# Performance work log

Measured on AMD Instinct MI355X. Metric: run time of the kernel, lower is better.

## Reference

```python
import jax, jax.numpy as jnp
import numpy as np

IN_F = 256
OUT_F = 256
ALPHA = 0.2  # leakyrelu negative slope


def setup_inputs() -> dict:
    key = jax.random.key(0)
    k1, k2, k3 = jax.random.split(key, 3)
    B, N = 64, 1024
    x_loc = jax.random.normal(k1, (B, N, IN_F), dtype=jnp.float32)
    # xavier_uniform with gain=1.414
    def xavier(k, shape, gain=1.414):
        fan_in, fan_out = shape[0], shape[1]
        bound = gain * np.sqrt(6.0 / (fan_in + fan_out))
        return jax.random.uniform(k, shape, jnp.float32, -bound, bound)
    W = xavier(k2, (IN_F, OUT_F))
    a = xavier(k3, (2 * OUT_F, 1))
    return {"x_loc": x_loc, "W": W, "a": a, "entity_num": N}


def reference(x_loc, W, a, entity_num):
    # h: [B, N, F]
    h = jnp.matmul(x_loc, W)
    F_out = W.shape[1]
    a1 = a[:F_out, 0]   # [F]
    a2 = a[F_out:, 0]   # [F]
    # score(i, j) = leakyrelu(a1 . h_i + a2 . h_j)  -- decomposition of
    # matmul(cat(h_i, h_j), a); identical math, avoids O(N^2 * 2F) tensor.
    s1 = jnp.einsum('bnf,f->bn', h, a1)  # [B, N]
    s2 = jnp.einsum('bnf,f->bn', h, a2)  # [B, N]
    e = s1[:, :, None] + s2[:, None, :]  # [B, N, N]
    e = jnp.where(e > 0, e, ALPHA * e)   # leakyrelu(alpha=0.2)
    attention = jax.nn.softmax(e, axis=2)
    h_prime = jnp.matmul(attention, h)   # [B, N, F]
    return h_prime  # concat=False -> no elu
```

## Files before the change

kernel.cpp:

```cpp
#include <hip/hip_runtime.h>


typedef unsigned short u16;
typedef unsigned int   u32;
typedef float  f32x4  __attribute__((ext_vector_type(4)));
typedef __bf16 bf16x8 __attribute__((ext_vector_type(8)));
typedef __bf16 bf16x4 __attribute__((ext_vector_type(4)));

#define NB    64
#define NENT  1024
#define FD    256
#define NROWS (NB * NENT)
#define ALPHA 0.2f

typedef __attribute__((address_space(1))) const void* gas_ptr;
typedef __attribute__((address_space(3))) void*       las_ptr;
__device__ __forceinline__ void gload16(const void* g, void* l) {
  __builtin_amdgcn_global_load_lds((gas_ptr)g, (las_ptr)l, 16, 0, 0);
}

__global__ __launch_bounds__(256) void k_wa(const float* __restrict__ W,
                                            const float* __restrict__ a,
                                            float* __restrict__ Wa1,
                                            float* __restrict__ Wa2) {
  const int k = blockIdx.x, f = threadIdx.x;
  const float w = W[(size_t)k * FD + f];
  float p1 = w * a[f];
  float p2 = w * a[FD + f];
#pragma unroll
  for (int off = 1; off < 64; off <<= 1) {
    p1 += __shfl_xor(p1, off, 64);
    p2 += __shfl_xor(p2, off, 64);
  }
  __shared__ float r1[4], r2[4];
  const int wv = f >> 6, lane = f & 63;
  if (lane == 0) { r1[wv] = p1; r2[wv] = p2; }
  __syncthreads();
  if (f == 0) {
    Wa1[k] = r1[0] + r1[1] + r1[2] + r1[3];
    Wa2[k] = r2[0] + r2[1] + r2[2] + r2[3];
  }
}

__global__ __launch_bounds__(256) void k_wt(const float* __restrict__ W,
                                            u16* __restrict__ Wt) {
  __shared__ float tile[64][65];
  const int t = threadIdx.x;
  const int ki = blockIdx.x >> 2, fi = blockIdx.x & 3;
  const int k0 = ki * 64, f0 = fi * 64;
  const int r = t >> 4, c4 = (t & 15) * 4;
#pragma unroll
  for (int it = 0; it < 4; ++it) {
    const int row = r + it * 16;
    float4 v = *(const float4*)&W[(size_t)(k0 + row) * FD + f0 + c4];
    tile[row][c4 + 0] = v.x; tile[row][c4 + 1] = v.y;
    tile[row][c4 + 2] = v.z; tile[row][c4 + 3] = v.w;
  }
  __syncthreads();
#pragma unroll
  for (int it = 0; it < 4; ++it) {
    const int fr = r + it * 16;
    bf16x4 pk;
    pk[0] = (__bf16)tile[c4 + 0][fr]; pk[1] = (__bf16)tile[c4 + 1][fr];
    pk[2] = (__bf16)tile[c4 + 2][fr]; pk[3] = (__bf16)tile[c4 + 3][fr];
    *(bf16x4*)&Wt[(size_t)(f0 + fr) * FD + k0 + c4] = pk;
  }
}

__global__ __launch_bounds__(512, 2) void k_h(
    const float* __restrict__ x, const u16* __restrict__ Wt,
    const float* __restrict__ Wa1g, const float* __restrict__ Wa2g,
    u16* __restrict__ h_oct, float* __restrict__ s1, float* __restrict__ s2) {
  __shared__ __align__(16) u16 A_lds[2][4][128][8];
  __shared__ __align__(16) u16 B_lds[2][4][256][8];
  __shared__ float wa1[FD], wa2[FD];
  const int t = threadIdx.x;
  const int lane = t & 63, wv = t >> 6;
  const int wr = wv >> 2, wc = wv & 3;
  const int g16 = lane >> 4, c15 = lane & 15;
  const int rT = blockIdx.x * 128;
  if (t < FD) { wa1[t] = Wa1g[t]; wa2[t] = Wa2g[t]; }
  const int srow = t >> 2, spart = t & 3;
  const float* xsrc = x + (size_t)(rT + srow) * FD + spart * 8;
  float p1 = 0.f, p2 = 0.f;
  f32x4 acc[4][4];
  const f32x4 vz = {0.f, 0.f, 0.f, 0.f};
#pragma unroll
  for (int i = 0; i < 4; ++i)
#pragma unroll
    for (int j = 0; j < 4; ++j) acc[i][j] = vz;

  auto stage = [&](int nb, int kc, const float4& f0, const float4& f1) {
    const int k0n = kc * 32;
    const int d0 = t;
    gload16(Wt + (size_t)(d0 & 255) * FD + k0n + (d0 >> 8) * 8,
            (char*)(&B_lds[nb][0][0][0]) + d0 * 16);
    const int d1 = t + 512;
    gload16(Wt + (size_t)(d1 & 255) * FD + k0n + (d1 >> 8) * 8,
            (char*)(&B_lds[nb][0][0][0]) + d1 * 16);
    bf16x8 aw;
    aw[0] = (__bf16)f0.x; aw[1] = (__bf16)f0.y;
    aw[2] = (__bf16)f0.z; aw[3] = (__bf16)f0.w;
    aw[4] = (__bf16)f1.x; aw[5] = (__bf16)f1.y;
    aw[6] = (__bf16)f1.z; aw[7] = (__bf16)f1.w;
    *(bf16x8*)&A_lds[nb][spart][srow][0] = aw;
    const int kb = k0n + spart * 8;
    p1 += f0.x*wa1[kb+0] + f0.y*wa1[kb+1] + f0.z*wa1[kb+2] + f0.w*wa1[kb+3]
        + f1.x*wa1[kb+4] + f1.y*wa1[kb+5] + f1.z*wa1[kb+6] + f1.w*wa1[kb+7];
    p2 += f0.x*wa2[kb+0] + f0.y*wa2[kb+1] + f0.z*wa2[kb+2] + f0.w*wa2[kb+3]
        + f1.x*wa2[kb+4] + f1.y*wa2[kb+5] + f1.z*wa2[kb+6] + f1.w*wa2[kb+7];
  };
  auto mfma_step = [&](int cb) {
    bf16x8 af[4], bfv[4];
#pragma unroll
    for (int fi = 0; fi < 4; ++fi)
      af[fi] = *(const bf16x8*)&A_lds[cb][g16][wr * 64 + fi * 16 + c15][0];
#pragma unroll
    for (int fj = 0; fj < 4; ++fj)
      bfv[fj] = *(const bf16x8*)&B_lds[cb][g16][wc * 64 + fj * 16 + c15][0];
#pragma unroll
    for (int fi = 0; fi < 4; ++fi)
#pragma unroll
      for (int fj = 0; fj < 4; ++fj)
        acc[fi][fj] = __builtin_amdgcn_mfma_f32_16x16x32_bf16(
            af[fi], bfv[fj], acc[fi][fj], 0, 0, 0);
  };

  float4 xc0 = *(const float4*)(xsrc + 0);
  float4 xc1 = *(const float4*)(xsrc + 4);
  float4 xb0 = *(const float4*)(xsrc + 32);
  float4 xb1 = *(const float4*)(xsrc + 36);
  float4 xa0 = *(const float4*)(xsrc + 64);
  float4 xa1 = *(const float4*)(xsrc + 68);
  __syncthreads();
  stage(0, 0, xc0, xc1);
  __syncthreads();
#pragma unroll 1
  for (int ks2 = 0; ks2 < 4; ++ks2) {
    stage(1, 2 * ks2 + 1, xb0, xb1);
    if (2 * ks2 + 3 < 8) {
      xb0 = *(const float4*)(xsrc + (2 * ks2 + 3) * 32);
      xb1 = *(const float4*)(xsrc + (2 * ks2 + 3) * 32 + 4);
    }
    mfma_step(0);
    __syncthreads();
    if (2 * ks2 + 2 < 8) {
      stage(0, 2 * ks2 + 2, xa0, xa1);
      if (2 * ks2 + 4 < 8) {
        xa0 = *(const float4*)(xsrc + (2 * ks2 + 4) * 32);
        xa1 = *(const float4*)(xsrc + (2 * ks2 + 4) * 32 + 4);
      }
    }
    mfma_step(1);
    __syncthreads();
  }
  p1 += __shfl_xor(p1, 1, 64); p1 += __shfl_xor(p1, 2, 64);
  p2 += __shfl_xor(p2, 1, 64); p2 += __shfl_xor(p2, 2, 64);
  if (spart == 0) { s1[rT + srow] = p1; s2[rT + srow] = p2; }
#pragma unroll
  for (int fi = 0; fi < 4; ++fi) {
    const int rowb = rT + wr * 64 + fi * 16 + 4 * g16;
    const int oct = rowb >> 3, u = rowb & 7;
#pragma unroll
    for (int fj = 0; fj < 4; ++fj) {
      const int col = wc * 64 + fj * 16 + c15;
      bf16x4 pk;
      pk[0] = (__bf16)acc[fi][fj][0]; pk[1] = (__bf16)acc[fi][fj][1];
      pk[2] = (__bf16)acc[fi][fj][2]; pk[3] = (__bf16)acc[fi][fj][3];
      *(bf16x4*)((u16*)h_oct + ((size_t)oct * FD + col) * 8 + u) = pk;
    }
  }
}

__global__ __launch_bounds__(512, 2) void k_pv(
    const u16* __restrict__ h_oct, const float* __restrict__ s1,
    const float* __restrict__ s2, float* __restrict__ out) {
  __shared__ __align__(16) u16 P_lds[2][4][128][8];
  __shared__ __align__(16) u16 V_lds[2][4][256][8];
  __shared__ float s2l[NENT];
  const int t = threadIdx.x;
  const int lane = t & 63, wv = t >> 6;
  const int wr = wv >> 2, wc = wv & 3;
  const int g16 = lane >> 4, c15 = lane & 15;
  const int p = blockIdx.x;
  const int lb = (p & 7) * 64 + (p >> 3);
  const int b = lb >> 3, itile = lb & 7;
  const int i0 = itile * 128;
  const int irow = t & 127, gsl = t >> 7;
  const int rowg = b * NENT + i0 + irow;
  const float s1v = s1[rowg];
  const size_t obase = (size_t)b * (NENT / 8);
  f32x4 acc[4][4];
  const f32x4 vz = {0.f, 0.f, 0.f, 0.f};
#pragma unroll
  for (int i = 0; i < 4; ++i)
#pragma unroll
    for (int j = 0; j < 4; ++j) acc[i][j] = vz;
  float zsum = 0.f;

  auto vload = [&](int nb, int ksn) {
    const int j0n = ksn * 32;
    const int d0 = t;
    gload16(h_oct + ((obase + (j0n >> 3) + (d0 >> 8)) * FD + (d0 & 255)) * 8,
            (char*)(&V_lds[nb][0][0][0]) + d0 * 16);
    const int d1 = t + 512;
    gload16(h_oct + ((obase + (j0n >> 3) + (d1 >> 8)) * FD + (d1 & 255)) * 8,
            (char*)(&V_lds[nb][0][0][0]) + d1 * 16);
  };

  vload(0, 0);
  *(float2*)&s2l[t * 2] = *(const float2*)&s2[(size_t)b * NENT + t * 2];
  __syncthreads();
  float sm = s2l[lane];
#pragma unroll
  for (int j = 1; j < 16; ++j) sm = fmaxf(sm, s2l[lane + j * 64]);
#pragma unroll
  for (int off = 1; off < 64; off <<= 1) sm = fmaxf(sm, __shfl_xor(sm, off, 64));
  const float q = s1v + sm;
  const float mv = fmaxf(q, ALPHA * q);

  auto genp = [&](int nb, int ksn) {
    const int jb = ksn * 32 + gsl * 8;
    bf16x8 pw;
    float zp = 0.f;
#pragma unroll
    for (int u = 0; u < 8; ++u) {
      float z = s1v + s2l[jb + u];
      float l = fmaxf(z, ALPHA * z);
      float pe = __expf(l - mv);
      zp += pe;
      pw[u] = (__bf16)pe;
    }
    zsum += zp;
    *(bf16x8*)&P_lds[nb][gsl][irow][0] = pw;
  };
  auto mfma_step = [&](int cb) {
    bf16x8 af[4], bfv[4];
#pragma unroll
    for (int fi = 0; fi < 4; ++fi)
      af[fi] = *(const bf16x8*)&P_lds[cb][g16][wr * 64 + fi * 16 + c15][0];
#pragma unroll
    for (int fj = 0; fj < 4; ++fj)
      bfv[fj] = *(const bf16x8*)&V_lds[cb][g16][wc * 64 + fj * 16 + c15][0];
#pragma unroll
    for (int fi = 0; fi < 4; ++fi)
#pragma unroll
      for (int fj = 0; fj < 4; ++fj)
        acc[fi][fj] = __builtin_amdgcn_mfma_f32_16x16x32_bf16(
            af[fi], bfv[fj], acc[fi][fj], 0, 0, 0);
  };

  genp(0, 0);
  __syncthreads();
#pragma unroll 1
  for (int ks2 = 0; ks2 < 16; ++ks2) {
    vload(1, 2 * ks2 + 1);
    genp(1, 2 * ks2 + 1);
    mfma_step(0);
    __syncthreads();
    if (2 * ks2 + 2 < 32) {
      vload(0, 2 * ks2 + 2);
      genp(0, 2 * ks2 + 2);
    }
    mfma_step(1);
    __syncthreads();
  }
  float* zred = (float*)&P_lds[0][0][0][0];
  zred[gsl * 128 + irow] = zsum;
  __syncthreads();
#pragma unroll
  for (int fi = 0; fi < 4; ++fi) {
    const int rowb = wr * 64 + fi * 16 + 4 * g16;
    float rz[4];
#pragma unroll
    for (int r = 0; r < 4; ++r)
      rz[r] = 1.0f / (zred[rowb + r] + zred[128 + rowb + r] +
                      zred[256 + rowb + r] + zred[384 + rowb + r]);
#pragma unroll
    for (int fj = 0; fj < 4; ++fj) {
      const int col = wc * 64 + fj * 16 + c15;
      float* o = out + ((size_t)b * NENT + i0 + rowb) * FD + col;
      o[0 * FD] = acc[fi][fj][0] * rz[0];
      o[1 * FD] = acc[fi][fj][1] * rz[1];
      o[2 * FD] = acc[fi][fj][2] * rz[2];
      o[3 * FD] = acc[fi][fj][3] * rz[3];
    }
  }
}

extern "C" void kernel_launch(void* const* d_in, const int* in_sizes, int n_in,
                              void* d_out, int out_size, void* d_ws, size_t ws_size,
                              hipStream_t stream) {
  const float* x = (const float*)d_in[0];
  const float* W = (const float*)d_in[1];
  const float* a = (const float*)d_in[2];
  float* out = (float*)d_out;

  char* ws = (char*)d_ws;
  u16*   h_oct = (u16*)ws;
  float* s1  = (float*)(ws + (size_t)33554432);
  float* s2  = s1 + NROWS;
  float* Wa1 = s2 + NROWS;
  float* Wa2 = Wa1 + FD;
  u16*   Wt  = (u16*)(Wa2 + FD);

  k_wa<<<dim3(256), dim3(256), 0, stream>>>(W, a, Wa1, Wa2);
  k_wt<<<dim3(16), dim3(256), 0, stream>>>(W, Wt);
  k_h<<<dim3(NROWS / 128), dim3(512), 0, stream>>>(x, Wt, Wa1, Wa2, h_oct, s1, s2);
  k_pv<<<dim3(NB * 8), dim3(512), 0, stream>>>(h_oct, s1, s2, out);
}
```

Baseline: 81.88 us.

## Double row tile to 256 in both GEMM kernels and use exp2-based softmax

Both k_h and k_pv now process 256 rows per block instead of 128, so each wave computes an 8x4 MFMA tile. This halves how often the W and V tiles are reloaded per output row and shrinks the grid to 256 blocks. The softmax generation in k_pv folds leakyrelu into a max of two FMAs followed by a raw v_exp_f32, and reads s2 with vector LDS loads. The larger accumulators raise register pressure, and the 256-block grid may leave compute units underused on a 256-CU device at 2 blocks per CU.

```diff
diff --git a/kernel.cpp b/kernel.cpp
--- a/kernel.cpp
+++ b/kernel.cpp
@@ -12,11 +12,17 @@
 #define FD    256
 #define NROWS (NB * NENT)
 #define ALPHA 0.2f
+#define LOG2E 1.4426950408889634f
 
 typedef __attribute__((address_space(1))) const void* gas_ptr;
 typedef __attribute__((address_space(3))) void*       las_ptr;
 __device__ __forceinline__ void gload16(const void* g, void* l) {
   __builtin_amdgcn_global_load_lds((gas_ptr)g, (las_ptr)l, 16, 0, 0);
+}
+__device__ __forceinline__ float fexp2(float x) {
+  float r;
+  asm("v_exp_f32 %0, %1" : "=v"(r) : "v"(x));
+  return r;
 }
 
 __global__ __launch_bounds__(256) void k_wa(const float* __restrict__ W,
@@ -71,26 +77,29 @@
     const float* __restrict__ x, const u16* __restrict__ Wt,
     const float* __restrict__ Wa1g, const float* __restrict__ Wa2g,
     u16* __restrict__ h_oct, float* __restrict__ s1, float* __restrict__ s2) {
-  __shared__ __align__(16) u16 A_lds[2][4][128][8];
+  __shared__ __align__(16) u16 A_lds[2][4][256][8];
   __shared__ __align__(16) u16 B_lds[2][4][256][8];
   __shared__ float wa1[FD], wa2[FD];
   const int t = threadIdx.x;
   const int lane = t & 63, wv = t >> 6;
   const int wr = wv >> 2, wc = wv & 3;
   const int g16 = lane >> 4, c15 = lane & 15;
-  const int rT = blockIdx.x * 128;
+  const int p = blockIdx.x;
+  const int lb = (p & 7) * 32 + (p >> 3);
+  const int rT = lb * 256;
   if (t < FD) { wa1[t] = Wa1g[t]; wa2[t] = Wa2g[t]; }
-  const int srow = t >> 2, spart = t & 3;
-  const float* xsrc = x + (size_t)(rT + srow) * FD + spart * 8;
+  const int row = t >> 1, half = t & 1;
+  const float* xsrc = x + (size_t)(rT + row) * FD + half * 16;
   float p1 = 0.f, p2 = 0.f;
-  f32x4 acc[4][4];
+  f32x4 acc[8][4];
   const f32x4 vz = {0.f, 0.f, 0.f, 0.f};
 #pragma unroll
-  for (int i = 0; i < 4; ++i)
+  for (int i = 0; i < 8; ++i)
 #pragma unroll
     for (int j = 0; j < 4; ++j) acc[i][j] = vz;
 
-  auto stage = [&](int nb, int kc, const float4& f0, const float4& f1) {
+  auto stage = [&](int nb, int kc, const float4& f0, const float4& f1,
+                   const float4& f2, const float4& f3) {
     const int k0n = kc * 32;
     const int d0 = t;
     gload16(Wt + (size_t)(d0 & 255) * FD + k0n + (d0 >> 8) * 8,
@@ -98,68 +107,84 @@
     const int d1 = t + 512;
     gload16(Wt + (size_t)(d1 & 255) * FD + k0n + (d1 >> 8) * 8,
             (char*)(&B_lds[nb][0][0][0]) + d1 * 16);
-    bf16x8 aw;
-    aw[0] = (__bf16)f0.x; aw[1] = (__bf16)f0.y;
-    aw[2] = (__bf16)f0.z; aw[3] = (__bf16)f0.w;
-    aw[4] = (__bf16)f1.x; aw[5] = (__bf16)f1.y;
-    aw[6] = (__bf16)f1.z; aw[7] = (__bf16)f1.w;
-    *(bf16x8*)&A_lds[nb][spart][srow][0] = aw;
-    const int kb = k0n + spart * 8;
-    p1 += f0.x*wa1[kb+0] + f0.y*wa1[kb+1] + f0.z*wa1[kb+2] + f0.w*wa1[kb+3]
-        + f1.x*wa1[kb+4] + f1.y*wa1[kb+5] + f1.z*wa1[kb+6] + f1.w*wa1[kb+7];
-    p2 += f0.x*wa2[kb+0] + f0.y*wa2[kb+1] + f0.z*wa2[kb+2] + f0.w*wa2[kb+3]
-        + f1.x*wa2[kb+4] + f1.y*wa2[kb+5] + f1.z*wa2[kb+6] + f1.w*wa2[kb+7];
+    bf16x8 w0, w1;
+    w0[0] = (__bf16)f0.x; w0[1] = (__bf16)f0.y;
+    w0[2] = (__bf16)f0.z; w0[3] = (__bf16)f0.w;
+    w0[4] = (__bf16)f1.x; w0[5] = (__bf16)f1.y;
+    w0[6] = (__bf16)f1.z; w0[7] = (__bf16)f1.w;
+    w1[0] = (__bf16)f2.x; w1[1] = (__bf16)f2.y;
+    w1[2] = (__bf16)f2.z; w1[3] = (__bf16)f2.w;
+    w1[4] = (__bf16)f3.x; w1[5] = (__bf16)f3.y;
+    w1[6] = (__bf16)f3.z; w1[7] = (__bf16)f3.w;
+    *(bf16x8*)&A_lds[nb][half * 2][row][0] = w0;
+    *(bf16x8*)&A_lds[nb][half * 2 + 1][row][0] = w1;
+    const int kb = k0n + half * 16;
+    p1 += f0.x*wa1[kb+ 0] + f0.y*wa1[kb+ 1] + f0.z*wa1[kb+ 2] + f0.w*wa1[kb+ 3]
+        + f1.x*wa1[kb+ 4] + f1.y*wa1[kb+ 5] + f1.z*wa1[kb+ 6] + f1.w*wa1[kb+ 7]
+        + f2.x*wa1[kb+ 8] + f2.y*wa1[kb+ 9] + f2.z*wa1[kb+10] + f2.w*wa1[kb+11]
+        + f3.x*wa1[kb+12] + f3.y*wa1[kb+13] + f3.z*wa1[kb+14] + f3.w*wa1[kb+15];
+    p2 += f0.x*wa2[kb+ 0] + f0.y*wa2[kb+ 1] + f0.z*wa2[kb+ 2] + f0.w*wa2[kb+ 3]
+        + f1.x*wa2[kb+ 4] + f1.y*wa2[kb+ 5] + f1.z*wa2[kb+ 6] + f1.w*wa2[kb+ 7]
+        + f2.x*wa2[kb+ 8] + f2.y*wa2[kb+ 9] + f2.z*wa2[kb+10] + f2.w*wa2[kb+11]
+        + f3.x*wa2[kb+12] + f3.y*wa2[kb+13] + f3.z*wa2[kb+14] + f3.w*wa2[kb+15];
   };
   auto mfma_step = [&](int cb) {
-    bf16x8 af[4], bfv[4];
-#pragma unroll
-    for (int fi = 0; fi < 4; ++fi)
-      af[fi] = *(const bf16x8*)&A_lds[cb][g16][wr * 64 + fi * 16 + c15][0];
+    bf16x8 bfv[4];
 #pragma unroll
     for (int fj = 0; fj < 4; ++fj)
       bfv[fj] = *(const bf16x8*)&B_lds[cb][g16][wc * 64 + fj * 16 + c15][0];
 #pragma unroll
-    for (int fi = 0; fi < 4; ++fi)
+    for (int fi = 0; fi < 8; ++fi) {
+      bf16x8 af = *(const bf16x8*)&A_lds[cb][g16][wr * 128 + fi * 16 + c15][0];
 #pragma unroll
       for (int fj = 0; fj < 4; ++fj)
         acc[fi][fj] = __builtin_amdgcn_mfma_f32_16x16x32_bf16(
-            af[fi], bfv[fj], acc[fi][fj], 0, 0, 0);
-  };
-
-  float4 xc0 = *(const float4*)(xsrc + 0);
-  float4 xc1 = *(const float4*)(xsrc + 4);
+            af, bfv[fj], acc[fi][fj], 0, 0, 0);
+    }
+  };
+
+  float4 xc0 = *(const float4*)(xsrc +  0);
+  float4 xc1 = *(const float4*)(xsrc +  4);
+  float4 xc2 = *(const float4*)(xsrc +  8);
+  float4 xc3 = *(const float4*)(xsrc + 12);
   float4 xb0 = *(const float4*)(xsrc + 32);
   float4 xb1 = *(const float4*)(xsrc + 36);
+  float4 xb2 = *(const float4*)(xsrc + 40);
+  float4 xb3 = *(const float4*)(xsrc + 44);
   float4 xa0 = *(const float4*)(xsrc + 64);
   float4 xa1 = *(const float4*)(xsrc + 68);
-  __syncthreads();
-  stage(0, 0, xc0, xc1);
+  float4 xa2 = *(const float4*)(xsrc + 72);
+  float4 xa3 = *(const float4*)(xsrc + 76);
+  __syncthreads();
+  stage(0, 0, xc0, xc1, xc2, xc3);
   __syncthreads();
 #pragma unroll 1
   for (int ks2 = 0; ks2 < 4; ++ks2) {
-    stage(1, 2 * ks2 + 1, xb0, xb1);
+    stage(1, 2 * ks2 + 1, xb0, xb1, xb2, xb3);
     if (2 * ks2 + 3 < 8) {
-      xb0 = *(const float4*)(xsrc + (2 * ks2 + 3) * 32);
-      xb1 = *(const float4*)(xsrc + (2 * ks2 + 3) * 32 + 4);
+      const float* s = xsrc + (2 * ks2 + 3) * 32;
+      xb0 = *(const float4*)(s);      xb1 = *(const float4*)(s + 4);
+      xb2 = *(const float4*)(s + 8);  xb3 = *(const float4*)(s + 12);
     }
     mfma_step(0);
     __syncthreads();
     if (2 * ks2 + 2 < 8) {
-      stage(0, 2 * ks2 + 2, xa0, xa1);
+      stage(0, 2 * ks2 + 2, xa0, xa1, xa2, xa3);
       if (2 * ks2 + 4 < 8) {
-        xa0 = *(const float4*)(xsrc + (2 * ks2 + 4) * 32);
-        xa1 = *(const float4*)(xsrc + (2 * ks2 + 4) * 32 + 4);
+        const float* s = xsrc + (2 * ks2 + 4) * 32;
+        xa0 = *(const float4*)(s);      xa1 = *(const float4*)(s + 4);
+        xa2 = *(const float4*)(s + 8);  xa3 = *(const float4*)(s + 12);
       }
     }
     mfma_step(1);
     __syncthreads();
   }
-  p1 += __shfl_xor(p1, 1, 64); p1 += __shfl_xor(p1, 2, 64);
-  p2 += __shfl_xor(p2, 1, 64); p2 += __shfl_xor(p2, 2, 64);
-  if (spart == 0) { s1[rT + srow] = p1; s2[rT + srow] = p2; }
-#pragma unroll
-  for (int fi = 0; fi < 4; ++fi) {
-    const int rowb = rT + wr * 64 + fi * 16 + 4 * g16;
+  p1 += __shfl_xor(p1, 1, 64);
+  p2 += __shfl_xor(p2, 1, 64);
+  if (half == 0) { s1[rT + row] = p1; s2[rT + row] = p2; }
+#pragma unroll
+  for (int fi = 0; fi < 8; ++fi) {
+    const int rowb = rT + wr * 128 + fi * 16 + 4 * g16;
     const int oct = rowb >> 3, u = rowb & 7;
 #pragma unroll
     for (int fj = 0; fj < 4; ++fj) {
@@ -175,7 +200,7 @@
 __global__ __launch_bounds__(512, 2) void k_pv(
     const u16* __restrict__ h_oct, const float* __restrict__ s1,
     const float* __restrict__ s2, float* __restrict__ out) {
-  __shared__ __align__(16) u16 P_lds[2][4][128][8];
+  __shared__ __align__(16) u16 P_lds[2][4][256][8];
   __shared__ __align__(16) u16 V_lds[2][4][256][8];
   __shared__ float s2l[NENT];
   const int t = threadIdx.x;
@@ -183,17 +208,17 @@
   const int wr = wv >> 2, wc = wv & 3;
   const int g16 = lane >> 4, c15 = lane & 15;
   const int p = blockIdx.x;
-  const int lb = (p & 7) * 64 + (p >> 3);
-  const int b = lb >> 3, itile = lb & 7;
-  const int i0 = itile * 128;
-  const int irow = t & 127, gsl = t >> 7;
+  const int lb = (p & 7) * 32 + (p >> 3);
+  const int b = lb >> 2, itile = lb & 3;
+  const int i0 = itile * 256;
+  const int irow = t & 255, gsl = t >> 8;
   const int rowg = b * NENT + i0 + irow;
   const float s1v = s1[rowg];
   const size_t obase = (size_t)b * (NENT / 8);
-  f32x4 acc[4][4];
+  f32x4 acc[8][4];
   const f32x4 vz = {0.f, 0.f, 0.f, 0.f};
 #pragma unroll
-  for (int i = 0; i < 4; ++i)
+  for (int i = 0; i < 8; ++i)
 #pragma unroll
     for (int j = 0; j < 4; ++j) acc[i][j] = vz;
   float zsum = 0.f;
@@ -218,36 +243,51 @@
   for (int off = 1; off < 64; off <<= 1) sm = fmaxf(sm, __shfl_xor(sm, off, 64));
   const float q = s1v + sm;
   const float mv = fmaxf(q, ALPHA * q);
+  const float C2v = ALPHA * LOG2E;
+  const float mvC = mv * LOG2E;
+  const float s1A = s1v * LOG2E - mvC;
+  const float s1B = s1v * C2v - mvC;
 
   auto genp = [&](int nb, int ksn) {
-    const int jb = ksn * 32 + gsl * 8;
-    bf16x8 pw;
+    const int jb = ksn * 32 + gsl * 16;
+    float4 qa = *(const float4*)&s2l[jb];
+    float4 qb = *(const float4*)&s2l[jb + 4];
+    float4 qc = *(const float4*)&s2l[jb + 8];
+    float4 qd = *(const float4*)&s2l[jb + 12];
     float zp = 0.f;
-#pragma unroll
-    for (int u = 0; u < 8; ++u) {
-      float z = s1v + s2l[jb + u];
-      float l = fmaxf(z, ALPHA * z);
-      float pe = __expf(l - mv);
-      zp += pe;
-      pw[u] = (__bf16)pe;
-    }
+    auto pg = [&](float s2j) -> float {
+      float vA = fmaf(s2j, LOG2E, s1A);
+      float vB = fmaf(s2j, C2v, s1B);
+      float r = fexp2(fmaxf(vA, vB));
+      zp += r;
+      return r;
+    };
+    bf16x8 pw0, pw1;
+    pw0[0] = (__bf16)pg(qa.x); pw0[1] = (__bf16)pg(qa.y);
+    pw0[2] = (__bf16)pg(qa.z); pw0[3] = (__bf16)pg(qa.w);
+    pw0[4] = (__bf16)pg(qb.x); pw0[5] = (__bf16)pg(qb.y);
+    pw0[6] = (__bf16)pg(qb.z); pw0[7] = (__bf16)pg(qb.w);
+    pw1[0] = (__bf16)pg(qc.x); pw1[1] = (__bf16)pg(qc.y);
+    pw1[2] = (__bf16)pg(qc.z); pw1[3] = (__bf16)pg(qc.w);
+    pw1[4] = (__bf16)pg(qd.x); pw1[5] = (__bf16)pg(qd.y);
+    pw1[6] = (__bf16)pg(qd.z); pw1[7] = (__bf16)pg(qd.w);
     zsum += zp;
-    *(bf16x8*)&P_lds[nb][gsl][irow][0] = pw;
+    *(bf16x8*)&P_lds[nb][2 * gsl][irow][0] = pw0;
+    *(bf16x8*)&P_lds[nb][2 * gsl + 1][irow][0] = pw1;
   };
   auto mfma_step = [&](int cb) {
-    bf16x8 af[4], bfv[4];
-#pragma unroll
-    for (int fi = 0; fi < 4; ++fi)
-      af[fi] = *(const bf16x8*)&P_lds[cb][g16][wr * 64 + fi * 16 + c15][0];
+    bf16x8 bfv[4];
 #pragma unroll
     for (int fj = 0; fj < 4; ++fj)
       bfv[fj] = *(const bf16x8*)&V_lds[cb][g16][wc * 64 + fj * 16 + c15][0];
 #pragma unroll
-    for (int fi = 0; fi < 4; ++fi)
+    for (int fi = 0; fi < 8; ++fi) {
+      bf16x8 af = *(const bf16x8*)&P_lds[cb][g16][wr * 128 + fi * 16 + c15][0];
 #pragma unroll
       for (int fj = 0; fj < 4; ++fj)
         acc[fi][fj] = __builtin_amdgcn_mfma_f32_16x16x32_bf16(
-            af[fi], bfv[fj], acc[fi][fj], 0, 0, 0);
+            af, bfv[fj], acc[fi][fj], 0, 0, 0);
+    }
   };
 
   genp(0, 0);
@@ -266,20 +306,19 @@
     __syncthreads();
   }
   float* zred = (float*)&P_lds[0][0][0][0];
-  zred[gsl * 128 + irow] = zsum;
-  __syncthreads();
-#pragma unroll
-  for (int fi = 0; fi < 4; ++fi) {
-    const int rowb = wr * 64 + fi * 16 + 4 * g16;
+  zred[gsl * 256 + irow] = zsum;
+  __syncthreads();
+#pragma unroll
+  for (int fi = 0; fi < 8; ++fi) {
+    const int rloc = wr * 128 + fi * 16 + 4 * g16;
     float rz[4];
 #pragma unroll
     for (int r = 0; r < 4; ++r)
-      rz[r] = 1.0f / (zred[rowb + r] + zred[128 + rowb + r] +
-                      zred[256 + rowb + r] + zred[384 + rowb + r]);
+      rz[r] = __builtin_amdgcn_rcpf(zred[rloc + r] + zred[256 + rloc + r]);
 #pragma unroll
     for (int fj = 0; fj < 4; ++fj) {
       const int col = wc * 64 + fj * 16 + c15;
-      float* o = out + ((size_t)b * NENT + i0 + rowb) * FD + col;
+      float* o = out + ((size_t)b * NENT + i0 + rloc) * FD + col;
       o[0 * FD] = acc[fi][fj][0] * rz[0];
       o[1 * FD] = acc[fi][fj][1] * rz[1];
       o[2 * FD] = acc[fi][fj][2] * rz[2];
@@ -306,6 +345,6 @@
 
   k_wa<<<dim3(256), dim3(256), 0, stream>>>(W, a, Wa1, Wa2);
   k_wt<<<dim3(16), dim3(256), 0, stream>>>(W, Wt);
-  k_h<<<dim3(NROWS / 128), dim3(512), 0, stream>>>(x, Wt, Wa1, Wa2, h_oct, s1, s2);
-  k_pv<<<dim3(NB * 8), dim3(512), 0, stream>>>(h_oct, s1, s2, out);
-}
+  k_h<<<dim3(256), dim3(512), 0, stream>>>(x, Wt, Wa1, Wa2, h_oct, s1, s2);
+  k_pv<<<dim3(256), dim3(512), 0, stream>>>(h_oct, s1, s2, out);
+}
```

After: 78.62 us. 1.04x faster.
